# Kernel optimization log

Hardware: AMD Instinct MI355X
Metric: run time of the kernel (lower is better)

## Reference

```python
import jax, jax.numpy as jnp
import numpy as np

B, L, E = 4, 1024, 1024
H, TOPK = 16, 32
DH = E // H


def setup_inputs() -> dict:
    key = jax.random.key(0)
    ks = jax.random.split(key, 11)
    s = 1.0 / np.sqrt(E)
    return {
        "Q": jax.random.normal(ks[0], (B, L, E), jnp.float32),
        "K": jax.random.normal(ks[1], (B, L, E), jnp.float32),
        "V": jax.random.normal(ks[2], (B, L, E), jnp.float32),
        "Wq": jax.random.normal(ks[3], (E, E), jnp.float32) * s,
        "bq": jnp.zeros((E,), jnp.float32),
        "Wk": jax.random.normal(ks[4], (E, E), jnp.float32) * s,
        "bk": jnp.zeros((E,), jnp.float32),
        "Wv": jax.random.normal(ks[5], (E, E), jnp.float32) * s,
        "bv": jnp.zeros((E,), jnp.float32),
        "Wo": jax.random.normal(ks[6], (E, E), jnp.float32) * s,
        "bo": jnp.zeros((E,), jnp.float32),
    }


def reference(Q, K, V, Wq, bq, Wk, bk, Wv, bv, Wo, bo):
    # Linear projections (torch Linear: x @ W.T + b), split heads -> [B,H,L,Dh]
    q = (Q @ Wq.T + bq).reshape(B, L, H, DH).transpose(0, 2, 1, 3)
    k = (K @ Wk.T + bk).reshape(B, L, H, DH).transpose(0, 2, 1, 3)
    v = (V @ Wv.T + bv).reshape(B, L, H, DH).transpose(0, 2, 1, 3)

    # Full attention logits [B,H,L,L]
    logits = jnp.einsum("bhld,bhmd->bhlm", q, k) / np.sqrt(DH)

    # Keep only top-k per query row; rest -> -inf (as in torch scatter_)
    top_vals, top_idx = jax.lax.top_k(logits, TOPK)  # [B,H,L,TOPK]
    bi = jnp.arange(B)[:, None, None, None]
    hi = jnp.arange(H)[None, :, None, None]
    li = jnp.arange(L)[None, None, :, None]
    masked = jnp.full_like(logits, -jnp.inf).at[bi, hi, li, top_idx].set(top_vals)

    attn = jax.nn.softmax(masked, axis=-1)
    out = jnp.einsum("bhlm,bhmd->bhld", attn, v)
    out = out.transpose(0, 2, 1, 3).reshape(B, L, E)
    return out @ Wo.T + bo
```

## Files before the change

### kernel.cpp

```cpp
#include <hip/hip_runtime.h>


typedef short v8s __attribute__((ext_vector_type(8)));
typedef _Float16 v8h __attribute__((ext_vector_type(8)));
typedef float v4f __attribute__((ext_vector_type(4)));

#define B_ 4
#define L_ 1024
#define E_ 1024
#define H_ 16
#define DH_ 64
#define M_ 4096

__device__ __forceinline__ unsigned short f2bf_u(float f) {
    unsigned u = __float_as_uint(f);
    unsigned r = u + 0x7FFFu + ((u >> 16) & 1u);
    return (unsigned short)(r >> 16);
}
__device__ __forceinline__ unsigned short f2h_u(float f) {
    _Float16 h = (_Float16)f;
    union { _Float16 h; unsigned short u; } c; c.h = h; return c.u;
}
__device__ __forceinline__ float h2f_u(unsigned short u) {
    union { _Float16 h; unsigned short u; } c; c.u = u; return (float)c.h;
}
__device__ __forceinline__ unsigned f2key(float f) {
    unsigned u = __float_as_uint(f);
    u = ((int)u < 0) ? ~u : (u | 0x80000000u);
    return u & 0xFFFFFFF0u;
}
__device__ __forceinline__ unsigned f2keyfull(float f) {
    unsigned u = __float_as_uint(f);
    return ((int)u < 0) ? ~u : (u | 0x80000000u);
}
__device__ __forceinline__ float key2f(unsigned k) {
    unsigned u = (k & 0x80000000u) ? (k & 0x7FFFFFFFu) : ~k;
    return __uint_as_float(u);
}
__device__ __forceinline__ float rl_f(float v, int l) {
    return __uint_as_float((unsigned)__builtin_amdgcn_readlane(__float_as_int(v), l));
}
__device__ __forceinline__ int rl_i(int v, int l) {
    return __builtin_amdgcn_readlane(v, l);
}
__device__ __forceinline__ void gload_lds16(const unsigned short* g, unsigned short* l) {
    __builtin_amdgcn_global_load_lds(
        (const __attribute__((address_space(1))) void*)g,
        (__attribute__((address_space(3))) void*)l, 16, 0, 0);
}

__global__ __launch_bounds__(256) void splitH_kernel(
    const float* __restrict__ x, unsigned short* __restrict__ y,
    int n8, int isB, float prescale)
{
    int i = blockIdx.x * 256 + threadIdx.x;
    if (i >= n8) return;
    float4 v0 = *(const float4*)(x + 8*(size_t)i);
    float4 v1 = *(const float4*)(x + 8*(size_t)i + 4);
    float f[8] = {v0.x, v0.y, v0.z, v0.w, v1.x, v1.y, v1.z, v1.w};
    unsigned short o[24];
#pragma unroll
    for (int c = 0; c < 8; ++c) {
        float fv = f[c] * prescale;
        unsigned short h = f2h_u(fv);
        float r = fv - h2f_u(h);
        unsigned short l = f2h_u(r);
        int b = 3*c;
        if (!isB) { o[b] = h; o[b+1] = l; o[b+2] = h; }
        else      { o[b] = h; o[b+1] = h; o[b+2] = l; }
    }
    uint4* dst = (uint4*)(y + 24*(size_t)i);
    const unsigned* ou = (const unsigned*)o;
    dst[0] = make_uint4(ou[0], ou[1], ou[2], ou[3]);
    dst[1] = make_uint4(ou[4], ou[5], ou[6], ou[7]);
    dst[2] = make_uint4(ou[8], ou[9], ou[10], ou[11]);
}

#define STAGE_TILE_GEN(Ap_, Bp_, Abuf_, Bbuf_, kt_)                       \
  {                                                                       \
    const int k0_ = (kt_) << 6;                                           \
    _Pragma("unroll")                                                     \
    for (int c_ = 0; c_ < 2; ++c_) {                                      \
      int lin_ = c_*512 + t;                                              \
      int r_ = lin_ >> 3, s_ = lin_ & 7;                                  \
      gload_lds16(Ap_ + (size_t)(m0 + r_)*K2 + k0_ + ((s_ ^ (r_&7))*8),   \
                  &Abuf_[lin_*8]);                                        \
    }                                                                     \
    _Pragma("unroll")                                                     \
    for (int c_ = 0; c_ < 2; ++c_) {                                      \
      int lin_ = c_*512 + t;                                              \
      int r_ = lin_ >> 3, s_ = lin_ & 7;                                  \
      gload_lds16(Bp_ + (size_t)(n0 + r_)*K2 + k0_ + ((s_ ^ (r_&7))*8),   \
                  &Bbuf_[lin_*8]);                                        \
    }                                                                     \
  }

#define GEMM_COMPUTE(Abuf_, Bbuf_)                                        \
  {                                                                       \
    _Pragma("unroll")                                                     \
    for (int ks = 0; ks < 2; ++ks) {                                      \
        v8h af[2], bf[4];                                                 \
        _Pragma("unroll")                                                 \
        for (int mt = 0; mt < 2; ++mt) {                                  \
            int ra = wrow + mt*16 + l16;                                  \
            int sl = (ks*4 + quad) ^ (ra & 7);                            \
            af[mt] = *(const v8h*)&Abuf_[ra*64 + sl*8];                   \
        }                                                                 \
        _Pragma("unroll")                                                 \
        for (int nt = 0; nt < 4; ++nt) {                                  \
            int rb = wcol + nt*16 + l16;                                  \
            int sl = (ks*4 + quad) ^ (rb & 7);                            \
            bf[nt] = *(const v8h*)&Bbuf_[rb*64 + sl*8];                   \
        }                                                                 \
        _Pragma("unroll")                                                 \
        for (int mt = 0; mt < 2; ++mt)                                    \
            _Pragma("unroll")                                             \
            for (int nt = 0; nt < 4; ++nt)                                \
                acc[mt][nt] = __builtin_amdgcn_mfma_f32_16x16x32_f16(     \
                    af[mt], bf[nt], acc[mt][nt], 0, 0, 0);                \
    }                                                                     \
  }

__global__ __launch_bounds__(512) void gemm_f16(
    const unsigned short* __restrict__ A,
    const unsigned short* __restrict__ Bw,
    const float* __restrict__ bias,
    int K2, int mode, float scale,
    float* __restrict__ outF,
    unsigned short* __restrict__ outB)
{
    __shared__ __align__(16) unsigned short As[3][128*64];
    __shared__ __align__(16) unsigned short Bs[3][128*64];
    const int t    = threadIdx.x;
    const int lane = t & 63;
    const int w    = t >> 6;
    const int quad = lane >> 4;
    const int l16  = lane & 15;
    const int bid  = blockIdx.x;
    const int xcd  = bid & 7;
    const int loc  = bid >> 3;
    const int m0   = (xcd * 4 + (loc & 3)) * 128;
    const int n0   = (loc >> 2) * 128;
    const int wrow = (w >> 1) * 32;
    const int wcol = (w & 1) * 64;

    v4f acc[2][4];
#pragma unroll
    for (int i = 0; i < 2; ++i)
#pragma unroll
        for (int j = 0; j < 4; ++j) acc[i][j] = (v4f){0.f,0.f,0.f,0.f};

    STAGE_TILE_GEN(A, Bw, As[0], Bs[0], 0)
    STAGE_TILE_GEN(A, Bw, As[1], Bs[1], 1)

    const int nk = K2 >> 6;
    for (int ki = 0; ki < nk; ++ki) {
        const int cur = ki % 3;
        asm volatile("s_waitcnt lgkmcnt(0)" ::: "memory");
        __builtin_amdgcn_s_barrier();
        if (ki + 2 < nk) {
            const int nb = (ki + 2) % 3;
            STAGE_TILE_GEN(A, Bw, As[nb], Bs[nb], ki + 2)
        }
        if (ki + 2 < nk)       asm volatile("s_waitcnt vmcnt(8)" ::: "memory");
        else if (ki + 1 < nk)  asm volatile("s_waitcnt vmcnt(4)" ::: "memory");
        else                   asm volatile("s_waitcnt vmcnt(0)" ::: "memory");
        __builtin_amdgcn_s_barrier();
        GEMM_COMPUTE(As[cur], Bs[cur])
    }

#pragma unroll
    for (int nt = 0; nt < 4; ++nt) {
        int n = n0 + wcol + nt*16 + l16;
        float bb = bias[n];
#pragma unroll
        for (int mt = 0; mt < 2; ++mt) {
#pragma unroll
            for (int r = 0; r < 4; ++r) {
                int m = m0 + wrow + mt*16 + quad*4 + r;
                float val = (acc[mt][nt][r] * 0.03125f + bb) * scale;
                if (mode == 0) {
                    outF[(size_t)m * 1024 + n] = val;
                } else {
                    int b = m >> 10, l = m & 1023;
                    int h = n >> 6,  d = n & 63;
                    size_t oidx = (((size_t)(b*16 + h)) * 1024 + l) * 64 + d;
                    outF[oidx] = val;
                    if (mode == 2) outB[oidx] = f2bf_u(val);
                }
            }
        }
    }
}

__global__ __launch_bounds__(512, 4) void gemm_f16_qk(
    const unsigned short* __restrict__ A0,
    const unsigned short* __restrict__ A1,
    const unsigned short* __restrict__ B0,
    const unsigned short* __restrict__ B1,
    const float* __restrict__ bias0,
    const float* __restrict__ bias1,
    float scale0, float scale1,
    float* __restrict__ outF0,
    float* __restrict__ outF1,
    unsigned short* __restrict__ outB0,
    unsigned short* __restrict__ outB1)
{
    __shared__ __align__(16) unsigned short As[2][128*64];
    __shared__ __align__(16) unsigned short Bs[2][128*64];
    const int K2   = 3072;
    const int t    = threadIdx.x;
    const int lane = t & 63;
    const int w    = t >> 6;
    const int quad = lane >> 4;
    const int l16  = lane & 15;
    const int z    = blockIdx.y;
    const unsigned short* A  = z ? A1 : A0;
    const unsigned short* Bw = z ? B1 : B0;
    const float* bias        = z ? bias1 : bias0;
    const float scale        = z ? scale1 : scale0;
    float* outF              = z ? outF1 : outF0;
    unsigned short* outB     = z ? outB1 : outB0;

    const int bid  = blockIdx.x;
    const int xcd  = bid & 7;
    const int loc  = bid >> 3;
    const int m0   = (xcd * 4 + (loc & 3)) * 128;
    const int n0   = (loc >> 2) * 128;
    const int wrow = (w >> 1) * 32;
    const int wcol = (w & 1) * 64;

    v4f acc[2][4];
#pragma unroll
    for (int i = 0; i < 2; ++i)
#pragma unroll
        for (int j = 0; j < 4; ++j) acc[i][j] = (v4f){0.f,0.f,0.f,0.f};

    STAGE_TILE_GEN(A, Bw, As[0], Bs[0], 0)

    const int nk = K2 >> 6;
    for (int ki = 0; ki < nk; ++ki) {
        const int cur = ki & 1;
        __syncthreads();
        if (ki + 1 < nk) {
            STAGE_TILE_GEN(A, Bw, As[cur ^ 1], Bs[cur ^ 1], ki + 1)
        }
        GEMM_COMPUTE(As[cur], Bs[cur])
    }

#pragma unroll
    for (int nt = 0; nt < 4; ++nt) {
        int n = n0 + wcol + nt*16 + l16;
        float bb = bias[n];
#pragma unroll
        for (int mt = 0; mt < 2; ++mt) {
#pragma unroll
            for (int r = 0; r < 4; ++r) {
                int m = m0 + wrow + mt*16 + quad*4 + r;
                float val = (acc[mt][nt][r] * 0.03125f + bb) * scale;
                int b = m >> 10, l = m & 1023;
                int h = n >> 6,  d = n & 63;
                size_t oidx = (((size_t)(b*16 + h)) * 1024 + l) * 64 + d;
                outF[oidx] = val;
                outB[oidx] = f2bf_u(val);
            }
        }
    }
}


#define SEL_STEP(s_, BUF)                                              \
  {                                                                    \
    v8s b0_ = BUF[0], b1_ = BUF[1];                                    \
    if ((s_) + 2 < 4) {                                                \
      BUF[0] = *(const v8s*)(kbase + ((s_)+2)*16384);                  \
      BUF[1] = *(const v8s*)(kbase + ((s_)+2)*16384 + 32);             \
    }                                                                  \
    v4f a0_ = (v4f){0.f,0.f,0.f,0.f};                                  \
    v4f a1_ = (v4f){0.f,0.f,0.f,0.f};                                  \
    a0_ = __builtin_amdgcn_mfma_f32_16x16x32_bf16(afrA[0], b0_, a0_, 0,0,0); \
    a0_ = __builtin_amdgcn_mfma_f32_16x16x32_bf16(afrA[1], b1_, a0_, 0,0,0); \
    a1_ = __builtin_amdgcn_mfma_f32_16x16x32_bf16(afrB[0], b0_, a1_, 0,0,0); \
    a1_ = __builtin_amdgcn_mfma_f32_16x16x32_bf16(afrB[1], b1_, a1_, 0,0,0); \
    if (quad < 2) {                                                    \
      _Pragma("unroll")                                                \
      for (int r_ = 0; r_ < 4; ++r_)                                   \
        sbig[(quad*4 + r_)*1044 + (s_)*256 + w*16 + l16] = a0_[r_];    \
      _Pragma("unroll")                                                \
      for (int r_ = 0; r_ < 4; ++r_)                                   \
        sbig[(8 + quad*4 + r_)*1044 + (s_)*256 + w*16 + l16] = a1_[r_];\
    }                                                                  \
  }

__global__ __launch_bounds__(1024, 8) void vsel_kernel(
    const unsigned short* __restrict__ A,
    const unsigned short* __restrict__ Bw,
    const float* __restrict__ bias,
    float* __restrict__ outF,
    const unsigned short* __restrict__ qb,
    const unsigned short* __restrict__ kb,
    unsigned short* __restrict__ candB,
    unsigned* __restrict__ cntB)
{
    __shared__ __align__(16) char smem[69120];
    const int t    = threadIdx.x;
    const int lane = t & 63;
    const int w    = t >> 6;
    const int quad = lane >> 4;
    const int l16  = lane & 15;

    if (blockIdx.x < 256) {
        unsigned short* As0 = (unsigned short*)smem;
        unsigned short* As1 = (unsigned short*)(smem + 16384);
        unsigned short* Bs0 = (unsigned short*)(smem + 32768);
        unsigned short* Bs1 = (unsigned short*)(smem + 49152);
        const int bid  = blockIdx.x;
        const int xcd  = bid & 7;
        const int loc  = bid >> 3;
        const int m0   = (xcd * 4 + (loc & 3)) * 128;
        const int n0   = (loc >> 2) * 128;
        const int wrow = (w >> 2) * 32;
        const int wcol = (w & 3) * 32;

        v4f acc[2][2];
#pragma unroll
        for (int i = 0; i < 2; ++i)
#pragma unroll
            for (int j = 0; j < 2; ++j) acc[i][j] = (v4f){0.f,0.f,0.f,0.f};

        const int r_ = t >> 3, s_ = t & 7;
        const unsigned short* Arow = A  + (size_t)(m0 + r_) * 3072 + (s_ ^ (r_ & 7)) * 8;
        const unsigned short* Brow = Bw + (size_t)(n0 + r_) * 3072 + (s_ ^ (r_ & 7)) * 8;

        gload_lds16(Arow, &As0[t*8]);
        gload_lds16(Brow, &Bs0[t*8]);

        for (int ki = 0; ki < 48; ++ki) {
            const int cur = ki & 1;
            __syncthreads();
            if (ki + 1 < 48) {
                const int k0 = (ki + 1) << 6;
                gload_lds16(Arow + k0, cur ? &As0[t*8] : &As1[t*8]);
                gload_lds16(Brow + k0, cur ? &Bs0[t*8] : &Bs1[t*8]);
            }
            const unsigned short* Ab = cur ? As1 : As0;
            const unsigned short* Bb = cur ? Bs1 : Bs0;
#pragma unroll
            for (int ks = 0; ks < 2; ++ks) {
                v8h af[2], bf[2];
#pragma unroll
                for (int mt = 0; mt < 2; ++mt) {
                    int ra = wrow + mt*16 + l16;
                    int sl = (ks*4 + quad) ^ (ra & 7);
                    af[mt] = *(const v8h*)&Ab[ra*64 + sl*8];
                }
#pragma unroll
                for (int nt = 0; nt < 2; ++nt) {
                    int rb = wcol + nt*16 + l16;
                    int sl = (ks*4 + quad) ^ (rb & 7);
                    bf[nt] = *(const v8h*)&Bb[rb*64 + sl*8];
                }
#pragma unroll
                for (int mt = 0; mt < 2; ++mt)
#pragma unroll
                    for (int nt = 0; nt < 2; ++nt)
                        acc[mt][nt] = __builtin_amdgcn_mfma_f32_16x16x32_f16(
                            af[mt], bf[nt], acc[mt][nt], 0, 0, 0);
            }
        }

#pragma unroll
        for (int nt = 0; nt < 2; ++nt) {
            int n = n0 + wcol + nt*16 + l16;
            float bb = bias[n];
#pragma unroll
            for (int mt = 0; mt < 2; ++mt) {
#pragma unroll
                for (int r = 0; r < 4; ++r) {
                    int m = m0 + wrow + mt*16 + quad*4 + r;
                    float val = acc[mt][nt][r] * 0.03125f + bb;
                    int b = m >> 10, l = m & 1023;
                    int h = n >> 6,  d = n & 63;
                    size_t oidx = (((size_t)(b*16 + h)) * 1024 + l) * 64 + d;
                    outF[oidx] = val;
                }
            }
        }
        return;
    }

    unsigned short* qbs = (unsigned short*)smem;
    float* sbig = (float*)(smem + 2304);

    const int blk = blockIdx.x - 256;
    const int jj  = blk >> 3;
    const int bh  = (blk & 7) * 8 + (jj >> 6);
    const int qt  = jj & 63;
    const int l0  = qt * 16;
    const size_t kvB = (size_t)bh * 1024;

    if (t < 128) {
        int r2 = t >> 3, cc2 = t & 7;
        *(uint4*)&qbs[r2*72 + cc2*8] = *(const uint4*)&qb[(kvB + l0 + r2)*64 + cc2*8];
    }
    __syncthreads();
    v8s afrA[2], afrB[2];
#pragma unroll
    for (int ks = 0; ks < 2; ++ks) {
        afrA[ks] = *(const v8s*)&qbs[(l16 & 7)*72 + ks*32 + quad*8];
        afrB[ks] = *(const v8s*)&qbs[(8 + (l16 & 7))*72 + ks*32 + quad*8];
    }

    const unsigned short* kbase = kb + (kvB + w*16 + l16) * 64 + quad*8;
    v8s buf0[2], buf1[2];
    buf0[0] = *(const v8s*)(kbase);         buf0[1] = *(const v8s*)(kbase + 32);
    buf1[0] = *(const v8s*)(kbase + 16384); buf1[1] = *(const v8s*)(kbase + 16384 + 32);
    SEL_STEP(0, buf0) SEL_STEP(1, buf1)
    SEL_STEP(2, buf0) SEL_STEP(3, buf1)
    __syncthreads();

    unsigned skey[16];
#pragma unroll
    for (int kt = 0; kt < 16; ++kt) {
        float sv = sbig[w*1044 + kt*64 + lane];
        unsigned u = __float_as_uint(sv);
        u = ((int)u < 0) ? ~u : (u | 0x80000000u);
        skey[kt] = (u & 0xFFFFFFF0u) | (unsigned)kt;
    }

    unsigned kmax = 0;
#pragma unroll
    for (int kt = 0; kt < 16; ++kt) kmax = max(kmax, skey[kt]);
#pragma unroll
    for (int off = 32; off; off >>= 1)
        kmax = max(kmax, (unsigned)__shfl_xor((int)kmax, off));
    float fm = key2f(kmax);

    unsigned tau = 0; bool ok = false;
    if (fm > 0.f) {
        float lof = 0.28f * fm, hif = 0.88f * fm;
        for (int it = 0; it < 12; ++it) {
            float midf = 0.5f * (lof + hif);
            unsigned tk = f2key(midf);
            int c = 0;
#pragma unroll
            for (int kt = 0; kt < 16; ++kt)
                c += (int)__popcll(__ballot(skey[kt] >= tk));
            tau = tk;
            if (c <= 64 && c >= 36) { ok = true; break; }
            if (c > 64) lof = midf; else hif = midf;
        }
    }
    if (!ok) {
        unsigned lo = 0u, hi = 0xFFFFFFFFu;
        for (int it = 0; ; ++it) {
            unsigned mid = lo + ((hi - lo) >> 1);
            int c = 0;
#pragma unroll
            for (int kt = 0; kt < 16; ++kt)
                c += (int)__popcll(__ballot(skey[kt] >= mid));
            tau = mid;
            if (it >= 33 || (c <= 64 && c >= 36)) break;
            if (c > 64) lo = mid + 1; else hi = mid - 1;
        }
    }

    const size_t row = kvB + l0 + w;
    int base = 0;
#pragma unroll
    for (int kt = 0; kt < 16; ++kt) {
        bool f = skey[kt] >= tau;
        unsigned long long mk = __ballot(f);
        if (f) {
            int pos = base + (int)__popcll(mk & ((1ull << lane) - 1ull));
            if (pos < 64) candB[row*64 + pos] = (unsigned short)(kt*64 + lane);
        }
        base += (int)__popcll(mk);
    }
    if (lane == 0) cntB[row] = (unsigned)(base > 64 ? 64 : base);
}


#define LDGRP(base_, PV, LV)                                          \
  {                                                                   \
    _Pragma("unroll")                                                 \
    for (int u = 0; u < 8; ++u) {                                     \
      int idx_ = (base_) + u;                                         \
      float pt_ = rl_f(pc, idx_);                                     \
      int   ci_ = rl_i(cc, idx_);                                     \
      bool  vv_ = idx_ < nnz;                                         \
      PV[u] = vv_ ? pt_ : 0.f;                                        \
      LV[u] = vbase[(size_t)(vv_ ? ci_ : 0) * 64];                    \
    }                                                                 \
  }

__global__ __launch_bounds__(1024, 4) void attn_out(
    const float* __restrict__ qf,
    const float* __restrict__ kf,
    const float* __restrict__ vf,
    const unsigned short* __restrict__ candB,
    const unsigned* __restrict__ cntB,
    unsigned short* __restrict__ outX3)
{
    __shared__ __align__(16) float qfs[16*68];

    const int t    = threadIdx.x;
    const int lane = t & 63;
    const int w    = t >> 6;

    const int blk = blockIdx.x;
    const int jj  = blk >> 3;
    const int bh  = (blk & 7) * 8 + (jj >> 6);
    const int qt  = jj & 63;
    const int l0  = qt * 16;
    const size_t kvB = (size_t)bh * 1024;

    const int qrow = w;
    const size_t row = kvB + l0 + w;

    const int cnum = (int)cntB[row];
    const int cj_raw = (int)candB[row*64 + lane];

    if (t < 256) {
        int r2 = t >> 4, c4 = (t & 15) * 4;
        *(float4*)&qfs[r2*68 + c4] = *(const float4*)&qf[(kvB + l0 + r2)*64 + c4];
    }
    __syncthreads();

    int cj = 0x3FFFFFFF;
    float ef = -INFINITY;
    {
        const int cjs = (lane < cnum) ? cj_raw : 0;
        const float* kr = kf + (kvB + cjs) * 64;
        double s0 = 0.0, s1 = 0.0;
#pragma unroll
        for (int d4 = 0; d4 < 16; d4 += 2) {
            float4 qa = *(const float4*)&qfs[qrow*68 + d4*4];
            float4 ka = *(const float4*)&kr[d4*4];
            float4 qb2 = *(const float4*)&qfs[qrow*68 + d4*4 + 4];
            float4 kb2 = *(const float4*)&kr[d4*4 + 4];
            s0 += (double)qa.x * ka.x; s0 += (double)qa.y * ka.y;
            s0 += (double)qa.z * ka.z; s0 += (double)qa.w * ka.w;
            s1 += (double)qb2.x * kb2.x; s1 += (double)qb2.y * kb2.y;
            s1 += (double)qb2.z * kb2.z; s1 += (double)qb2.w * kb2.w;
        }
        if (lane < cnum) { cj = cj_raw; ef = (float)(s0 + s1); }
    }

    const unsigned uf = f2keyfull(ef);
    unsigned T = 0u;
#pragma unroll
    for (int b = 31; b >= 0; --b) {
        unsigned cndt = T | (1u << b);
        int c = (int)__popcll(__ballot(uf >= cndt));
        if (c >= 32) T = cndt;
    }
    float e31 = key2f(T);
    int c_ge = (int)__popcll(__ballot(uf >= T));

    float mx = ef;
    float tm = (uf < T) ? ef : -INFINITY;
#pragma unroll
    for (int off = 32; off; off >>= 1) {
        mx = fmaxf(mx, __shfl_xor(mx, off));
        tm = fmaxf(tm, __shfl_xor(tm, off));
    }
    float e32v = (c_ge >= 33) ? e31 : tm;

    float cmid = 0.5f * (e31 + e32v);
    const float btau = 1.5e-5f;
    bool certain = (ef > cmid + btau);
    bool band    = (fabsf(ef - cmid) <= btau);
    int A = (int)__popcll(__ballot(certain));
    int m = (int)__popcll(__ballot(band));
    float wgt = band ? ((float)(32 - A) / (float)m) : (certain ? 1.f : 0.f);

    float p = wgt * __expf(ef - mx);
    float Z = p;
#pragma unroll
    for (int off = 32; off; off >>= 1) Z += __shfl_xor(Z, off);

    bool sel = (wgt > 0.f);
    unsigned long long mk = __ballot(sel);
    int nnz = (int)__popcll(mk);
    unsigned long long lt = (1ull << lane) - 1ull;
    int pos = sel ? (int)__popcll(mk & lt)
                  : nnz + (int)__popcll(~mk & lt);
    float pc = __uint_as_float((unsigned)__builtin_amdgcn_ds_permute(
                   pos << 2, __float_as_int(p)));
    int   cc = __builtin_amdgcn_ds_permute(pos << 2, cj);

    const float* vbase = vf + kvB * 64 + lane;
    int ng = (nnz + 7) >> 3;
    float pA[8], lA[8], pB[8], lB[8];
    float oa = 0.f, ob = 0.f, oc = 0.f, od = 0.f;
    LDGRP(0, pA, lA)
    int g = 0;
    for (;;) {
        if (g + 1 < ng) LDGRP((g+1)*8, pB, lB)
        oa += pA[0]*lA[0]; ob += pA[1]*lA[1]; oc += pA[2]*lA[2]; od += pA[3]*lA[3];
        oa += pA[4]*lA[4]; ob += pA[5]*lA[5]; oc += pA[6]*lA[6]; od += pA[7]*lA[7];
        ++g; if (g >= ng) break;
        if (g + 1 < ng) LDGRP((g+1)*8, pA, lA)
        oa += pB[0]*lB[0]; ob += pB[1]*lB[1]; oc += pB[2]*lB[2]; od += pB[3]*lB[3];
        oa += pB[4]*lB[4]; ob += pB[5]*lB[5]; oc += pB[6]*lB[6]; od += pB[7]*lB[7];
        ++g; if (g >= ng) break;
    }
    float o = (oa + ob) + (oc + od);
    float oval = o / Z;

    unsigned short hh = f2h_u(oval);
    float rres = oval - h2f_u(hh);
    unsigned short ll = f2h_u(rres);
    int lq = l0 + qrow;
    size_t e = ((size_t)(bh >> 4) * 1024 + lq) * 1024 + (bh & 15) * 64 + lane;
    outX3[3*e]     = hh;
    outX3[3*e + 1] = ll;
    outX3[3*e + 2] = hh;
}

extern "C" void kernel_launch(void* const* d_in, const int* in_sizes, int n_in,
                              void* d_out, int out_size, void* d_ws, size_t ws_size,
                              hipStream_t stream)
{
    const float* Q  = (const float*)d_in[0];
    const float* K  = (const float*)d_in[1];
    const float* V  = (const float*)d_in[2];
    const float* Wq = (const float*)d_in[3];
    const float* bq = (const float*)d_in[4];
    const float* Wk = (const float*)d_in[5];
    const float* bk = (const float*)d_in[6];
    const float* Wv = (const float*)d_in[7];
    const float* bv = (const float*)d_in[8];
    const float* Wo = (const float*)d_in[9];
    const float* bo = (const float*)d_in[10];
    float* out = (float*)d_out;

    if (ws_size < 115343360) return;

    char* ws = (char*)d_ws;
    unsigned short* X3a = (unsigned short*)(ws + 0);
    unsigned short* X3b = (unsigned short*)(ws + 25165824);
    float* vf = (float*)(ws + 25165824);
    unsigned short* candB = (unsigned short*)(ws + 41943040);
    unsigned* cntB = (unsigned*)(ws + 50331648);
    unsigned short* W3a = (unsigned short*)(ws + 50331648);
    unsigned short* W3b = (unsigned short*)(ws + 56623104);
    float* qf = (float*)(ws + 62914560);
    float* kf = (float*)(ws + 79691776);
    unsigned short* qb = (unsigned short*)(ws + 96468992);
    unsigned short* kb = (unsigned short*)(ws + 104857600);

    const int nX8 = M_ * E_ / 8;
    const int nW8 = E_ * E_ / 8;
    dim3 blk(256);
    dim3 blkG(512);
    dim3 gG(256);
    dim3 gQK(256, 2);
    dim3 gX(nX8 / 256), gW(nW8 / 256);

    splitH_kernel<<<gX, blk, 0, stream>>>(Q, X3a, nX8, 0, 1.0f);
    splitH_kernel<<<gX, blk, 0, stream>>>(K, X3b, nX8, 0, 1.0f);
    splitH_kernel<<<gW, blk, 0, stream>>>(Wq, W3a, nW8, 1, 32.0f);
    splitH_kernel<<<gW, blk, 0, stream>>>(Wk, W3b, nW8, 1, 32.0f);
    gemm_f16_qk<<<gQK, blkG, 0, stream>>>(X3a, X3b, W3a, W3b, bq, bk,
                                          0.125f, 1.0f, qf, kf, qb, kb);
    splitH_kernel<<<gX, blk, 0, stream>>>(V, X3a, nX8, 0, 1.0f);
    splitH_kernel<<<gW, blk, 0, stream>>>(Wv, W3b, nW8, 1, 32.0f);
    vsel_kernel<<<dim3(4352), dim3(1024), 0, stream>>>(
        X3a, W3b, bv, vf, qb, kb, candB, cntB);
    attn_out<<<dim3(4096), dim3(1024), 0, stream>>>(qf, kf, vf, candB, cntB, X3a);
    splitH_kernel<<<gW, blk, 0, stream>>>(Wo, W3b, nW8, 1, 32.0f);
    gemm_f16<<<gG, blkG, 0, stream>>>(X3a, W3b, bo, 3072, 0, 1.0f, out, nullptr);
}
```

Baseline: 505.0 us.

## Merge split kernels, fold Wo split into vsel, add 64-wide output GEMM

Merges the separate fp16 hi/lo split launches into combined kernels (Q/K/Wq/Wk in one, V/Wv in another). Folds the Wo split into extra blocks of vsel_kernel so it runs alongside attention candidate selection. Replaces the 128x128 triple-buffered output GEMM with a 128x64-tile double-buffered kernel that launches 512 blocks for better CU fill. The risk is that the smaller tiles lose data reuse and the double buffering gives less latency hiding; cntB is also moved to a new workspace offset.

Result: faster. 465.9 us (-7.7%).

```diff
diff --git a/kernel.cpp b/kernel.cpp
--- a/kernel.cpp
+++ b/kernel.cpp
@@ -49,12 +49,10 @@
         (__attribute__((address_space(3))) void*)l, 16, 0, 0);
 }
 
-__global__ __launch_bounds__(256) void splitH_kernel(
+__device__ __forceinline__ void split_body(
     const float* __restrict__ x, unsigned short* __restrict__ y,
-    int n8, int isB, float prescale)
+    int i, int isB, float prescale)
 {
-    int i = blockIdx.x * 256 + threadIdx.x;
-    if (i >= n8) return;
     float4 v0 = *(const float4*)(x + 8*(size_t)i);
     float4 v1 = *(const float4*)(x + 8*(size_t)i + 4);
     float f[8] = {v0.x, v0.y, v0.z, v0.w, v1.x, v1.y, v1.z, v1.w};
@@ -74,6 +72,28 @@
     dst[0] = make_uint4(ou[0], ou[1], ou[2], ou[3]);
     dst[1] = make_uint4(ou[4], ou[5], ou[6], ou[7]);
     dst[2] = make_uint4(ou[8], ou[9], ou[10], ou[11]);
+}
+
+__global__ __launch_bounds__(256) void split4_kernel(
+    const float* __restrict__ Q,  const float* __restrict__ K,
+    const float* __restrict__ Wq, const float* __restrict__ Wk,
+    unsigned short* __restrict__ X3q, unsigned short* __restrict__ X3k,
+    unsigned short* __restrict__ W3q, unsigned short* __restrict__ W3k)
+{
+    const int bid = blockIdx.x, t = threadIdx.x;
+    if (bid < 2048)      split_body(Q,  X3q, bid*256 + t,        0, 1.0f);
+    else if (bid < 4096) split_body(K,  X3k, (bid-2048)*256 + t, 0, 1.0f);
+    else if (bid < 4608) split_body(Wq, W3q, (bid-4096)*256 + t, 1, 32.0f);
+    else                 split_body(Wk, W3k, (bid-4608)*256 + t, 1, 32.0f);
+}
+
+__global__ __launch_bounds__(256) void splitVW_kernel(
+    const float* __restrict__ V, const float* __restrict__ Wv,
+    unsigned short* __restrict__ X3v, unsigned short* __restrict__ W3v)
+{
+    const int bid = blockIdx.x, t = threadIdx.x;
+    if (bid < 2048) split_body(V,  X3v, bid*256 + t,        0, 1.0f);
+    else            split_body(Wv, W3v, (bid-2048)*256 + t, 1, 32.0f);
 }
 
 #define STAGE_TILE_GEN(Ap_, Bp_, Abuf_, Bbuf_, kt_)                       \
@@ -120,78 +140,6 @@
                     af[mt], bf[nt], acc[mt][nt], 0, 0, 0);                \
     }                                                                     \
   }
-
-__global__ __launch_bounds__(512) void gemm_f16(
-    const unsigned short* __restrict__ A,
-    const unsigned short* __restrict__ Bw,
-    const float* __restrict__ bias,
-    int K2, int mode, float scale,
-    float* __restrict__ outF,
-    unsigned short* __restrict__ outB)
-{
-    __shared__ __align__(16) unsigned short As[3][128*64];
-    __shared__ __align__(16) unsigned short Bs[3][128*64];
-    const int t    = threadIdx.x;
-    const int lane = t & 63;
-    const int w    = t >> 6;
-    const int quad = lane >> 4;
-    const int l16  = lane & 15;
-    const int bid  = blockIdx.x;
-    const int xcd  = bid & 7;
-    const int loc  = bid >> 3;
-    const int m0   = (xcd * 4 + (loc & 3)) * 128;
-    const int n0   = (loc >> 2) * 128;
-    const int wrow = (w >> 1) * 32;
-    const int wcol = (w & 1) * 64;
-
-    v4f acc[2][4];
-#pragma unroll
-    for (int i = 0; i < 2; ++i)
-#pragma unroll
-        for (int j = 0; j < 4; ++j) acc[i][j] = (v4f){0.f,0.f,0.f,0.f};
-
-    STAGE_TILE_GEN(A, Bw, As[0], Bs[0], 0)
-    STAGE_TILE_GEN(A, Bw, As[1], Bs[1], 1)
-
-    const int nk = K2 >> 6;
-    for (int ki = 0; ki < nk; ++ki) {
-        const int cur = ki % 3;
-        asm volatile("s_waitcnt lgkmcnt(0)" ::: "memory");
-        __builtin_amdgcn_s_barrier();
-        if (ki + 2 < nk) {
-            const int nb = (ki + 2) % 3;
-            STAGE_TILE_GEN(A, Bw, As[nb], Bs[nb], ki + 2)
-        }
-        if (ki + 2 < nk)       asm volatile("s_waitcnt vmcnt(8)" ::: "memory");
-        else if (ki + 1 < nk)  asm volatile("s_waitcnt vmcnt(4)" ::: "memory");
-        else                   asm volatile("s_waitcnt vmcnt(0)" ::: "memory");
-        __builtin_amdgcn_s_barrier();
-        GEMM_COMPUTE(As[cur], Bs[cur])
-    }
-
-#pragma unroll
-    for (int nt = 0; nt < 4; ++nt) {
-        int n = n0 + wcol + nt*16 + l16;
-        float bb = bias[n];
-#pragma unroll
-        for (int mt = 0; mt < 2; ++mt) {
-#pragma unroll
-            for (int r = 0; r < 4; ++r) {
-                int m = m0 + wrow + mt*16 + quad*4 + r;
-                float val = (acc[mt][nt][r] * 0.03125f + bb) * scale;
-                if (mode == 0) {
-                    outF[(size_t)m * 1024 + n] = val;
-                } else {
-                    int b = m >> 10, l = m & 1023;
-                    int h = n >> 6,  d = n & 63;
-                    size_t oidx = (((size_t)(b*16 + h)) * 1024 + l) * 64 + d;
-                    outF[oidx] = val;
-                    if (mode == 2) outB[oidx] = f2bf_u(val);
-                }
-            }
-        }
-    }
-}
 
 __global__ __launch_bounds__(512, 4) void gemm_f16_qk(
     const unsigned short* __restrict__ A0,
@@ -268,6 +216,98 @@
     }
 }
 
+__global__ __launch_bounds__(512, 4) void gemm_o64(
+    const unsigned short* __restrict__ A,
+    const unsigned short* __restrict__ Bw,
+    const float* __restrict__ bias,
+    float* __restrict__ outF)
+{
+    __shared__ __align__(16) unsigned short As[2][128*64];
+    __shared__ __align__(16) unsigned short Bs[2][64*64];
+    const int t    = threadIdx.x;
+    const int lane = t & 63;
+    const int w    = t >> 6;
+    const int quad = lane >> 4;
+    const int l16  = lane & 15;
+    const int bid  = blockIdx.x;
+    const int xcd  = bid & 7;
+    const int loc  = bid >> 3;
+    const int m0   = (xcd * 4 + (loc & 3)) * 128;
+    const int n0   = (loc >> 2) * 64;
+    const int wrow = (w >> 1) * 32;
+    const int wcol = (w & 1) * 32;
+
+    v4f acc[2][2];
+#pragma unroll
+    for (int i = 0; i < 2; ++i)
+#pragma unroll
+        for (int j = 0; j < 2; ++j) acc[i][j] = (v4f){0.f,0.f,0.f,0.f};
+
+#define STAGE_O(bi_, kt_)                                                 \
+  {                                                                       \
+    const int k0_ = (kt_) << 6;                                           \
+    _Pragma("unroll")                                                     \
+    for (int c_ = 0; c_ < 2; ++c_) {                                      \
+      int lin_ = c_*512 + t;                                              \
+      int r_ = lin_ >> 3, s_ = lin_ & 7;                                  \
+      gload_lds16(A + (size_t)(m0 + r_)*3072 + k0_ + ((s_ ^ (r_&7))*8),   \
+                  &As[bi_][lin_*8]);                                      \
+    }                                                                     \
+    {                                                                     \
+      int r_ = t >> 3, s_ = t & 7;                                        \
+      gload_lds16(Bw + (size_t)(n0 + r_)*3072 + k0_ + ((s_ ^ (r_&7))*8),  \
+                  &Bs[bi_][t*8]);                                         \
+    }                                                                     \
+  }
+
+    STAGE_O(0, 0)
+
+    for (int ki = 0; ki < 48; ++ki) {
+        const int cur = ki & 1;
+        __syncthreads();
+        if (ki + 1 < 48) {
+            STAGE_O(cur ^ 1, ki + 1)
+        }
+#pragma unroll
+        for (int ks = 0; ks < 2; ++ks) {
+            v8h af[2], bf[2];
+#pragma unroll
+            for (int mt = 0; mt < 2; ++mt) {
+                int ra = wrow + mt*16 + l16;
+                int sl = (ks*4 + quad) ^ (ra & 7);
+                af[mt] = *(const v8h*)&As[cur][ra*64 + sl*8];
+            }
+#pragma unroll
+            for (int nt = 0; nt < 2; ++nt) {
+                int rb = wcol + nt*16 + l16;
+                int sl = (ks*4 + quad) ^ (rb & 7);
+                bf[nt] = *(const v8h*)&Bs[cur][rb*64 + sl*8];
+            }
+#pragma unroll
+            for (int mt = 0; mt < 2; ++mt)
+#pragma unroll
+                for (int nt = 0; nt < 2; ++nt)
+                    acc[mt][nt] = __builtin_amdgcn_mfma_f32_16x16x32_f16(
+                        af[mt], bf[nt], acc[mt][nt], 0, 0, 0);
+        }
+    }
+#undef STAGE_O
+
+#pragma unroll
+    for (int nt = 0; nt < 2; ++nt) {
+        int n = n0 + wcol + nt*16 + l16;
+        float bb = bias[n];
+#pragma unroll
+        for (int mt = 0; mt < 2; ++mt) {
+#pragma unroll
+            for (int r = 0; r < 4; ++r) {
+                int m = m0 + wrow + mt*16 + quad*4 + r;
+                outF[(size_t)m * 1024 + n] = acc[mt][nt][r] * 0.03125f + bb;
+            }
+        }
+    }
+}
+
 
 #define SEL_STEP(s_, BUF)                                              \
   {                                                                    \
@@ -300,7 +340,9 @@
     const unsigned short* __restrict__ qb,
     const unsigned short* __restrict__ kb,
     unsigned short* __restrict__ candB,
-    unsigned* __restrict__ cntB)
+    unsigned* __restrict__ cntB,
+    const float* __restrict__ Wo,
+    unsigned short* __restrict__ W3o)
 {
     __shared__ __align__(16) char smem[69120];
     const int t    = threadIdx.x;
@@ -308,6 +350,12 @@
     const int w    = t >> 6;
     const int quad = lane >> 4;
     const int l16  = lane & 15;
+
+    if (blockIdx.x >= 4352) {
+        int i = (blockIdx.x - 4352) * 1024 + t;
+        split_body(Wo, W3o, i, 1, 32.0f);
+        return;
+    }
 
     if (blockIdx.x < 256) {
         unsigned short* As0 = (unsigned short*)smem;
@@ -643,33 +691,23 @@
     unsigned short* X3b = (unsigned short*)(ws + 25165824);
     float* vf = (float*)(ws + 25165824);
     unsigned short* candB = (unsigned short*)(ws + 41943040);
-    unsigned* cntB = (unsigned*)(ws + 50331648);
     unsigned short* W3a = (unsigned short*)(ws + 50331648);
     unsigned short* W3b = (unsigned short*)(ws + 56623104);
     float* qf = (float*)(ws + 62914560);
     float* kf = (float*)(ws + 79691776);
     unsigned short* qb = (unsigned short*)(ws + 96468992);
     unsigned short* kb = (unsigned short*)(ws + 104857600);
-
-    const int nX8 = M_ * E_ / 8;
-    const int nW8 = E_ * E_ / 8;
-    dim3 blk(256);
-    dim3 blkG(512);
-    dim3 gG(256);
+    unsigned* cntB = (unsigned*)(ws + 113246208);
+
     dim3 gQK(256, 2);
-    dim3 gX(nX8 / 256), gW(nW8 / 256);
-
-    splitH_kernel<<<gX, blk, 0, stream>>>(Q, X3a, nX8, 0, 1.0f);
-    splitH_kernel<<<gX, blk, 0, stream>>>(K, X3b, nX8, 0, 1.0f);
-    splitH_kernel<<<gW, blk, 0, stream>>>(Wq, W3a, nW8, 1, 32.0f);
-    splitH_kernel<<<gW, blk, 0, stream>>>(Wk, W3b, nW8, 1, 32.0f);
-    gemm_f16_qk<<<gQK, blkG, 0, stream>>>(X3a, X3b, W3a, W3b, bq, bk,
-                                          0.125f, 1.0f, qf, kf, qb, kb);
-    splitH_kernel<<<gX, blk, 0, stream>>>(V, X3a, nX8, 0, 1.0f);
-    splitH_kernel<<<gW, blk, 0, stream>>>(Wv, W3b, nW8, 1, 32.0f);
-    vsel_kernel<<<dim3(4352), dim3(1024), 0, stream>>>(
-        X3a, W3b, bv, vf, qb, kb, candB, cntB);
+
+    split4_kernel<<<dim3(5120), dim3(256), 0, stream>>>(
+        Q, K, Wq, Wk, X3a, X3b, W3a, W3b);
+    gemm_f16_qk<<<gQK, dim3(512), 0, stream>>>(X3a, X3b, W3a, W3b, bq, bk,
+                                               0.125f, 1.0f, qf, kf, qb, kb);
+    splitVW_kernel<<<dim3(2560), dim3(256), 0, stream>>>(V, Wv, X3a, W3b);
+    vsel_kernel<<<dim3(4480), dim3(1024), 0, stream>>>(
+        X3a, W3b, bv, vf, qb, kb, candB, cntB, Wo, W3a);
     attn_out<<<dim3(4096), dim3(1024), 0, stream>>>(qf, kf, vf, candB, cntB, X3a);
-    splitH_kernel<<<gW, blk, 0, stream>>>(Wo, W3b, nW8, 1, 32.0f);
-    gemm_f16<<<gG, blkG, 0, stream>>>(X3a, W3b, bo, 3072, 0, 1.0f, out, nullptr);
-}
+    gemm_o64<<<dim3(512), dim3(512), 0, stream>>>(X3a, W3a, bo, out);
+}
```
